# Performance work log

Hardware: AMD Instinct MI355X
Metric: run time of the kernel (lower is better)

The kernel has to match this reference:

```python
import jax, jax.numpy as jnp
import numpy as np

HW = 256  # fixed UV/image resolution hardcoded in the module


def _grid_sample_nearest(inp, grid):
    """torch.F.grid_sample(mode='nearest', padding_mode='zeros', align_corners=False).
    inp: [N,C,H,W], grid: [N,Hg,Wg,2] with (x,y) in [-1,1]. Returns [N,C,Hg,Wg]."""
    N, C, H, W = inp.shape
    x = grid[..., 0]
    y = grid[..., 1]
    # align_corners=False pixel mapping
    ix = jnp.round(((x + 1.0) * W - 1.0) * 0.5).astype(jnp.int32)
    iy = jnp.round(((y + 1.0) * H - 1.0) * 0.5).astype(jnp.int32)
    valid = (ix >= 0) & (ix < W) & (iy >= 0) & (iy < H)
    ixc = jnp.clip(ix, 0, W - 1)
    iyc = jnp.clip(iy, 0, H - 1)
    gathered = jax.vmap(lambda im, yy, xx: im[:, yy, xx])(inp, iyc, ixc)  # [N,C,Hg,Wg]
    return gathered * valid[:, None, :, :].astype(inp.dtype)


def setup_inputs() -> dict:
    key = jax.random.key(0)
    k1, k2, k3, k4 = jax.random.split(key, 4)
    bs = 128
    grid = jax.random.uniform(k1, (bs, 2, HW, HW), jnp.float32, -1.0, 1.0)
    seg = jax.random.uniform(k2, (bs, 1, HW, HW), jnp.float32)
    conf_is = jax.random.uniform(k3, (bs, 1, HW, HW), jnp.float32)
    depth = jax.random.normal(k4, (bs, 1, HW, HW), jnp.float32)
    return {"grid": grid, "seg": seg, "conf_is": conf_is, "depth": depth}


def reference(grid, seg, conf_is, depth):
    bs = grid.shape[0]
    # segmentation mask with all-True fallback for empty masks
    seg_mask = seg > 0.5  # [bs,1,H,W] bool
    n_valid = jnp.sum(seg_mask, axis=(1, 2, 3))
    seg_mask = jnp.where((n_valid == 0)[:, None, None, None], True, seg_mask)

    gridm = grid * seg_mask  # bool broadcast over channel dim
    grid_int = ((gridm + 1.0) * 0.5 * HW).astype(jnp.int32)  # trunc-toward-zero == torch .long()
    grid_int = jnp.clip(grid_int, 0, HW - 1)

    # meshgrid_uv[h, w] = [w, h]
    hh, ww = jnp.meshgrid(jnp.arange(HW), jnp.arange(HW), indexing='ij')
    mesh_uv = jnp.stack([ww, hh], axis=-1).astype(jnp.float32)  # [H,W,2]

    # per-batch scatter write: grid_uv[b, gy, gx] = mesh_uv  (the irregular-access hot spot)
    def scatter_one(gy, gx):
        return jnp.zeros((HW, HW, 2), jnp.float32).at[gy, gx].set(mesh_uv)

    grid_uv = jax.vmap(scatter_one)(grid_int[:, 1], grid_int[:, 0])  # [bs,H,W,2]
    grid_uv = grid_uv / 128.0 - 1.0

    mesh_x = jnp.broadcast_to((ww / 280.0).astype(jnp.float32)[None, None], (bs, 1, HW, HW))
    mesh_y = jnp.broadcast_to((hh / 280.0).astype(jnp.float32)[None, None], (bs, 1, HW, HW))
    dkpt_img = jnp.concatenate([mesh_x, mesh_y, depth], axis=1) * seg_mask  # [bs,3,H,W]

    dkpt_uv = _grid_sample_nearest(dkpt_img, grid_uv)           # [bs,3,H,W]
    conf_is_uv = _grid_sample_nearest(conf_is, grid_uv)          # [bs,1,H,W]
    mask_uv = _grid_sample_nearest(seg_mask.astype(jnp.float32), grid_uv)[:, 0]  # [bs,H,W]
    return dkpt_uv, conf_is_uv, mask_uv
```

## Files before the change

### kernel.cpp

```cpp
#include <hip/hip_runtime.h>

#define HW    256
#define HW2   65536
#define BS    128
#define NT    1024
#define QPB   16384
#define QQ    4096

__global__ __launch_bounds__(NT, 8) void fused_kernel(
        const float* __restrict__ grid,
        const float* __restrict__ seg,
        const float* __restrict__ conf,
        const float* __restrict__ depth,
        float* __restrict__ out) {
    __shared__ unsigned int Wl[HW2 / 4];
    __shared__ unsigned long long segbits[4][256];
    __shared__ int red[16];
    __shared__ int flag_s;

    const int b       = blockIdx.x & (BS - 1);
    const int quarter = blockIdx.x >> 7;
    const int tid  = threadIdx.x;
    const int wave = tid >> 6;
    const int lane = tid & 63;

    const float* segb   = seg   + (size_t)b * HW2;
    const float* confb  = conf  + (size_t)b * HW2;
    const float* depthb = depth + (size_t)b * HW2;

    {
        uint4* Wz = (uint4*)Wl;
        #pragma unroll
        for (int k = 0; k < 4; ++k) Wz[tid + k * NT] = make_uint4(0u, 0u, 0u, 0u);
    }
    unsigned long long mbits = 0ULL;
    int cnt = 0;
    {
        const float4* s4 = (const float4*)segb;
        #pragma unroll
        for (int k = 0; k < 16; ++k) {
            int i = tid + k * NT;
            float4 v = s4[i];
            bool px = v.x > 0.5f, py = v.y > 0.5f, pz = v.z > 0.5f, pw = v.w > 0.5f;
            unsigned long long bx = __ballot(px);
            unsigned long long by = __ballot(py);
            unsigned long long bz = __ballot(pz);
            unsigned long long bw = __ballot(pw);
            if (lane == 0) {
                int wi = wave + k * 16;
                segbits[0][wi] = bx; segbits[1][wi] = by;
                segbits[2][wi] = bz; segbits[3][wi] = bw;
                cnt += __popcll(bx) + __popcll(by) + __popcll(bz) + __popcll(bw);
            }
            unsigned long long q = (px ? 1ULL : 0ULL) | (py ? 2ULL : 0ULL) |
                                   (pz ? 4ULL : 0ULL) | (pw ? 8ULL : 0ULL);
            mbits |= q << (k * 4);
        }
    }
    if (lane == 0) red[wave] = cnt;
    __syncthreads();
    if (tid == 0) {
        int t = 0;
        #pragma unroll
        for (int w = 0; w < 16; ++w) t += red[w];
        flag_s = (t == 0) ? 1 : 0;
    }
    __syncthreads();
    const int flagb = flag_s;

    {
        const float4* gx4 = (const float4*)(grid + (size_t)(2 * b) * HW2);
        const float4* gy4 = (const float4*)(grid + (size_t)(2 * b + 1) * HW2);
        int masked_max = -1;
        #pragma unroll 4
        for (int k = 0; k < 16; ++k) {
            int i = tid + k * NT;
            float4 X = gx4[i];
            float4 Y = gy4[i];
            int hw0 = i * 4;
            float xa[4] = {X.x, X.y, X.z, X.w};
            float ya[4] = {Y.x, Y.y, Y.z, Y.w};
            #pragma unroll
            for (int j = 0; j < 4; ++j) {
                bool m = flagb || ((mbits >> (k * 4 + j)) & 1ULL);
                if (m) {
                    float fx = (xa[j] + 1.0f) * 0.5f * 256.0f;
                    float fy = (ya[j] + 1.0f) * 0.5f * 256.0f;
                    int gxi = min(max((int)fx, 0), HW - 1);
                    int gyi = min(max((int)fy, 0), HW - 1);
                    if ((gyi >> 6) == quarter)
                        atomicMax(&Wl[(gyi & 63) * HW + gxi], (unsigned int)(hw0 + j));
                } else {
                    masked_max = hw0 + j;
                }
            }
        }
        int mm = masked_max;
        for (int off = 32; off > 0; off >>= 1) mm = max(mm, __shfl_xor(mm, off));
        if (quarter == 2 && lane == 0 && mm >= 0)
            atomicMax(&Wl[(128 & 63) * HW + 128], (unsigned int)mm);
    }
    __syncthreads();

    float4* out4 = (float4*)out;
    const size_t dkBase = (size_t)(b * 3) * QPB;
    const size_t O1q = (size_t)BS * 3 * QPB + (size_t)b * QPB;
    const size_t O2q = (size_t)BS * 4 * QPB + (size_t)b * QPB;
    #pragma unroll 4
    for (int k = 0; k < 4; ++k) {
        int i = tid + k * NT;
        uint4 wv = ((const uint4*)Wl)[i];
        unsigned la[4] = {wv.x, wv.y, wv.z, wv.w};
        float o0[4], o1[4], o2[4], oc[4], om[4];
        #pragma unroll
        for (int j = 0; j < 4; ++j) {
            unsigned l = la[j];
            int ix = (int)(l & 255u) & ~1;
            int iy = (int)(l >> 8) & ~1;
            int off = iy * HW + ix;
            int q = off >> 2;
            float m;
            if (flagb) m = 1.0f;
            else       m = (float)((segbits[off & 3][q >> 6] >> (q & 63)) & 1ULL);
            o0[j] = ((float)ix / 280.0f) * m;
            o1[j] = ((float)iy / 280.0f) * m;
            o2[j] = depthb[off] * m;
            oc[j] = confb[off];
            om[j] = m;
        }
        size_t gq = (size_t)quarter * QQ + i;
        out4[dkBase + gq]           = make_float4(o0[0], o0[1], o0[2], o0[3]);
        out4[dkBase + QPB + gq]     = make_float4(o1[0], o1[1], o1[2], o1[3]);
        out4[dkBase + 2 * QPB + gq] = make_float4(o2[0], o2[1], o2[2], o2[3]);
        out4[O1q + gq]              = make_float4(oc[0], oc[1], oc[2], oc[3]);
        out4[O2q + gq]              = make_float4(om[0], om[1], om[2], om[3]);
    }
}

extern "C" void kernel_launch(void* const* d_in, const int* in_sizes, int n_in,
                              void* d_out, int out_size, void* d_ws, size_t ws_size,
                              hipStream_t stream) {
    const float* grid  = (const float*)d_in[0];
    const float* seg   = (const float*)d_in[1];
    const float* conf  = (const float*)d_in[2];
    const float* depth = (const float*)d_in[3];
    float* out = (float*)d_out;
    fused_kernel<<<BS * 4, NT, 0, stream>>>(grid, seg, conf, depth, out);
}
```

Baseline: 319.3 us.

## Split fused kernel into half-image scatter with 16-bit LDS table and gather pass

```diff
diff --git a/kernel.cpp b/kernel.cpp
--- a/kernel.cpp
+++ b/kernel.cpp
@@ -3,10 +3,196 @@
 #define HW    256
 #define HW2   65536
 #define BS    128
-#define NT    1024
+#define NTS   1024
 #define QPB   16384
-#define QQ    4096
-
+#define HQ    8192
+
+
+__device__ __forceinline__ void lds_max_u16(unsigned int* W32, int cell, unsigned int val) {
+    unsigned int* word = W32 + (cell >> 1);
+    unsigned int sh = (cell & 1) << 4;
+    unsigned int assumed = *word;
+    while (((assumed >> sh) & 0xFFFFu) < val) {
+        unsigned int nw = (assumed & ~(0xFFFFu << sh)) | (val << sh);
+        unsigned int prev = atomicCAS(word, assumed, nw);
+        if (prev == assumed) break;
+        assumed = prev;
+    }
+}
+
+__global__ __launch_bounds__(NTS, 1) void scatter_kernel(
+        const float* __restrict__ grid,
+        const float* __restrict__ seg,
+        const float* __restrict__ conf,
+        const float* __restrict__ depth,
+        unsigned short* __restrict__ W16,
+        float4* __restrict__ packed) {
+    __shared__ unsigned short Wl[HW2];
+    __shared__ int red[16];
+    __shared__ int flag_s;
+
+    const int b    = blockIdx.x & (BS - 1);
+    const int h    = blockIdx.x >> 7;
+    const int tid  = threadIdx.x;
+    const int wave = tid >> 6;
+    const int lane = tid & 63;
+    unsigned int* W32 = (unsigned int*)Wl;
+
+    const float* segb   = seg   + (size_t)b * HW2;
+    const float* confb  = conf  + (size_t)b * HW2;
+    const float* depthb = depth + (size_t)b * HW2;
+
+    {
+        uint4* Wz = (uint4*)W32;
+        #pragma unroll
+        for (int k = 0; k < 8; ++k) Wz[tid + k * NTS] = make_uint4(0u, 0u, 0u, 0u);
+    }
+    unsigned int mbits = 0u;
+    int cnt = 0;
+    {
+        const float4* s4 = (const float4*)segb;
+        #pragma unroll
+        for (int k = 0; k < 8; ++k) {
+            float4 v = s4[h * HQ + tid + k * NTS];
+            unsigned q = (v.x > 0.5f ? 1u : 0u) | (v.y > 0.5f ? 2u : 0u) |
+                         (v.z > 0.5f ? 4u : 0u) | (v.w > 0.5f ? 8u : 0u);
+            mbits |= q << (k * 4);
+            cnt += __popc(q);
+        }
+        #pragma unroll
+        for (int k = 0; k < 8; ++k) {
+            float4 v = s4[(1 - h) * HQ + tid + k * NTS];
+            cnt += (v.x > 0.5f) + (v.y > 0.5f) + (v.z > 0.5f) + (v.w > 0.5f);
+        }
+    }
+    for (int off = 32; off > 0; off >>= 1) cnt += __shfl_down(cnt, off);
+    if (lane == 0) red[wave] = cnt;
+    __syncthreads();
+    if (tid == 0) {
+        int t = 0;
+        #pragma unroll
+        for (int w = 0; w < 16; ++w) t += red[w];
+        flag_s = (t == 0) ? 1 : 0;
+    }
+    __syncthreads();
+    const int flagb = flag_s;
+
+    {
+        const float4* gx4 = (const float4*)(grid + (size_t)(2 * b) * HW2);
+        const float4* gy4 = (const float4*)(grid + (size_t)(2 * b + 1) * HW2);
+        int masked_max = -1;
+        #pragma unroll 4
+        for (int k = 0; k < 8; ++k) {
+            int i = h * HQ + tid + k * NTS;
+            float4 X = gx4[i];
+            float4 Y = gy4[i];
+            int hw0 = i * 4;
+            float xa[4] = {X.x, X.y, X.z, X.w};
+            float ya[4] = {Y.x, Y.y, Y.z, Y.w};
+            #pragma unroll
+            for (int j = 0; j < 4; ++j) {
+                bool m = flagb || ((mbits >> (k * 4 + j)) & 1u);
+                if (m) {
+                    float fx = (xa[j] + 1.0f) * 0.5f * 256.0f;
+                    float fy = (ya[j] + 1.0f) * 0.5f * 256.0f;
+                    int gxi = min(max((int)fx, 0), HW - 1);
+                    int gyi = min(max((int)fy, 0), HW - 1);
+                    lds_max_u16(W32, gyi * HW + gxi, (unsigned int)(hw0 + j));
+                } else {
+                    masked_max = hw0 + j;
+                }
+            }
+        }
+        int mm = masked_max;
+        for (int off = 32; off > 0; off >>= 1) mm = max(mm, __shfl_xor(mm, off));
+        if (lane == 0 && mm >= 0)
+            lds_max_u16(W32, 128 * HW + 128, (unsigned int)mm);
+    }
+
+    {
+        float4* packb = packed + (size_t)b * 16384;
+        #pragma unroll
+        for (int rr = 0; rr < 4; ++rr) {
+            int rl = wave * 4 + rr;
+            int r  = 128 * h + 2 * rl;
+            int qr = r * 64 + lane;
+            float4 d = ((const float4*)depthb)[qr];
+            float4 c = ((const float4*)confb)[qr];
+            float4 s = ((const float4*)segb)[qr];
+            float m0 = (flagb || s.x > 0.5f) ? 1.0f : 0.0f;
+            float m1 = (flagb || s.z > 0.5f) ? 1.0f : 0.0f;
+            int p = (r >> 1) * 128 + 2 * lane;
+            packb[p]     = make_float4(d.x * m0, c.x, m0, 0.0f);
+            packb[p + 1] = make_float4(d.z * m1, c.z, m1, 0.0f);
+        }
+    }
+    __syncthreads();
+
+    {
+        unsigned short* Wout = W16 + ((size_t)h * BS + b) * HW2;
+        const uint4* Wl4 = (const uint4*)Wl;
+        #pragma unroll
+        for (int k = 0; k < 8; ++k)
+            ((uint4*)Wout)[tid + k * NTS] = Wl4[tid + k * NTS];
+    }
+}
+
+__global__ __launch_bounds__(256, 8) void gather_kernel(
+        const unsigned short* __restrict__ W16,
+        const float4* __restrict__ packed,
+        float* __restrict__ out) {
+    __shared__ float lut[128];
+    if (threadIdx.x < 128) lut[threadIdx.x] = (float)(2 * threadIdx.x) / 280.0f;
+    __syncthreads();
+
+    const int B   = blockIdx.x;
+    const int xcd = B & 7;
+    const int k   = B >> 3;
+    const int b   = (k & 15) * 8 + xcd;
+    const int s   = k >> 4;
+    const int q0  = s * 1024;
+
+    const unsigned short* W0 = W16 + (size_t)b * HW2;
+    const unsigned short* W1 = W16 + ((size_t)BS + b) * HW2;
+    const float4* packb = packed + (size_t)b * 16384;
+    float4* out4 = (float4*)out;
+    const size_t dkBase = (size_t)(b * 3) * QPB;
+    const size_t O1 = (size_t)BS * 3 * QPB + (size_t)b * QPB;
+    const size_t O2 = (size_t)BS * 4 * QPB + (size_t)b * QPB;
+
+    #pragma unroll
+    for (int t = 0; t < 4; ++t) {
+        int q = q0 + threadIdx.x + t * 256;
+        uint2 a  = ((const uint2*)W0)[q];
+        uint2 c2 = ((const uint2*)W1)[q];
+        unsigned la[4] = { max(a.x & 0xFFFFu, c2.x & 0xFFFFu),
+                           max(a.x >> 16,     c2.x >> 16),
+                           max(a.y & 0xFFFFu, c2.y & 0xFFFFu),
+                           max(a.y >> 16,     c2.y >> 16) };
+        float o0[4], o1[4], o2v[4], oc[4], om[4];
+        #pragma unroll
+        for (int j = 0; j < 4; ++j) {
+            unsigned l = la[j];
+            int ix = (int)(l & 255u) & ~1;
+            int iy = (int)(l >> 8) & ~1;
+            float4 p = packb[(iy >> 1) * 128 + (ix >> 1)];
+            float m = p.z;
+            o0[j]  = lut[ix >> 1] * m;
+            o1[j]  = lut[iy >> 1] * m;
+            o2v[j] = p.x;
+            oc[j]  = p.y;
+            om[j]  = m;
+        }
+        out4[dkBase + q]           = make_float4(o0[0], o0[1], o0[2], o0[3]);
+        out4[dkBase + QPB + q]     = make_float4(o1[0], o1[1], o1[2], o1[3]);
+        out4[dkBase + 2 * QPB + q] = make_float4(o2v[0], o2v[1], o2v[2], o2v[3]);
+        out4[O1 + q]               = make_float4(oc[0], oc[1], oc[2], oc[3]);
+        out4[O2 + q]               = make_float4(om[0], om[1], om[2], om[3]);
+    }
+}
+
+#define NT 1024
+#define QQ 4096
 __global__ __launch_bounds__(NT, 8) void fused_kernel(
         const float* __restrict__ grid,
         const float* __restrict__ seg,
@@ -17,17 +203,14 @@
     __shared__ unsigned long long segbits[4][256];
     __shared__ int red[16];
     __shared__ int flag_s;
-
     const int b       = blockIdx.x & (BS - 1);
     const int quarter = blockIdx.x >> 7;
     const int tid  = threadIdx.x;
     const int wave = tid >> 6;
     const int lane = tid & 63;
-
     const float* segb   = seg   + (size_t)b * HW2;
     const float* confb  = conf  + (size_t)b * HW2;
     const float* depthb = depth + (size_t)b * HW2;
-
     {
         uint4* Wz = (uint4*)Wl;
         #pragma unroll
@@ -42,10 +225,8 @@
             int i = tid + k * NT;
             float4 v = s4[i];
             bool px = v.x > 0.5f, py = v.y > 0.5f, pz = v.z > 0.5f, pw = v.w > 0.5f;
-            unsigned long long bx = __ballot(px);
-            unsigned long long by = __ballot(py);
-            unsigned long long bz = __ballot(pz);
-            unsigned long long bw = __ballot(pw);
+            unsigned long long bx = __ballot(px), by = __ballot(py);
+            unsigned long long bz = __ballot(pz), bw = __ballot(pw);
             if (lane == 0) {
                 int wi = wave + k * 16;
                 segbits[0][wi] = bx; segbits[1][wi] = by;
@@ -67,7 +248,6 @@
     }
     __syncthreads();
     const int flagb = flag_s;
-
     {
         const float4* gx4 = (const float4*)(grid + (size_t)(2 * b) * HW2);
         const float4* gy4 = (const float4*)(grid + (size_t)(2 * b + 1) * HW2);
@@ -101,7 +281,6 @@
             atomicMax(&Wl[(128 & 63) * HW + 128], (unsigned int)mm);
     }
     __syncthreads();
-
     float4* out4 = (float4*)out;
     const size_t dkBase = (size_t)(b * 3) * QPB;
     const size_t O1q = (size_t)BS * 3 * QPB + (size_t)b * QPB;
@@ -145,5 +324,15 @@
     const float* conf  = (const float*)d_in[2];
     const float* depth = (const float*)d_in[3];
     float* out = (float*)d_out;
-    fused_kernel<<<BS * 4, NT, 0, stream>>>(grid, seg, conf, depth, out);
-}
+
+    const size_t W16Bytes  = (size_t)2 * BS * HW2 * sizeof(unsigned short);
+    const size_t packBytes = (size_t)BS * 16384 * sizeof(float4);
+    if (ws_size >= W16Bytes + packBytes) {
+        unsigned short* W16 = (unsigned short*)d_ws;
+        float4* packed = (float4*)((char*)d_ws + W16Bytes);
+        scatter_kernel<<<BS * 2, NTS, 0, stream>>>(grid, seg, conf, depth, W16, packed);
+        gather_kernel<<<2048, 256, 0, stream>>>(W16, packed, out);
+    } else {
+        fused_kernel<<<BS * 4, NT, 0, stream>>>(grid, seg, conf, depth, out);
+    }
+}
```

After: 329.8 us. 3.3% more time.
